# Kernel tuning notes

Hardware: AMD Instinct MI355X
Metric: run time of the kernel (lower is better)

## Reference

```python
import jax, jax.numpy as jnp
import numpy as np

N_NODES = 10000
N_EDGES = 320000
K_HOPS = 3
IN_CH = 128
OUT_CH = 128


def setup_inputs() -> dict:
    key = jax.random.key(0)
    k1, k2, k3, k4, k5 = jax.random.split(key, 5)
    h = jax.random.normal(k1, (N_NODES, IN_CH), dtype=jnp.float32)
    X = jax.random.normal(k2, (N_EDGES, K_HOPS), dtype=jnp.float32)
    edge_index = jax.random.randint(k3, (2, N_EDGES), 0, N_NODES, dtype=jnp.int64)
    batch_node = jax.random.uniform(k4, (N_NODES,), dtype=jnp.float32)
    # glorot init for weight, zeros for bias (matches reset_parameters)
    stdv = np.sqrt(6.0 / (IN_CH + OUT_CH))
    weight = jax.random.uniform(k5, (K_HOPS, IN_CH, OUT_CH), dtype=jnp.float32,
                                minval=-stdv, maxval=stdv)
    bias = jnp.zeros((OUT_CH,), dtype=jnp.float32)
    return {"h": h, "X": X, "edge_index": edge_index,
            "batch_node": batch_node, "weight": weight, "bias": bias}


def reference(h, X, edge_index, batch_node, weight, bias):
    # Original builds dense A[k, src, dst] = X[e, k] (zeros elsewhere), then
    # res = A @ h @ weight, max over k, + bias. We honor the sparsity:
    # agg[src, k, :] = sum_e X[e, k] * h[dst[e], :]  (sparse A @ h per hop k)
    n = batch_node.shape[0]
    src = edge_index[0]
    dst = edge_index[1]
    msg = X[:, :, None] * h[dst][:, None, :]                 # [E, K, in]
    agg = jax.ops.segment_sum(msg, src, num_segments=n)      # [N, K, in]
    res = jnp.einsum('nki,kio->kno', agg, weight)            # [K, N, out]
    out = res.max(axis=0) + bias                             # [N, out]
    return out
```

## Files before the change

kernel.cpp:

```cpp
#include <hip/hip_runtime.h>

#define N_NODES 10000
#define N_EDGES 320000
#define K_HOPS  3
#define CH      128
#define NBF     4
#define ROWP    136
#define SLOT    72

#define EDGE_BLKS 1250
#define HCV_BLKS  1250
#define WCV_BLKS  192

typedef __attribute__((ext_vector_type(8))) short  frag8;
typedef __attribute__((ext_vector_type(4))) float  floatx4;

__device__ inline unsigned short f2bf(float x) {
    union { float f; unsigned u; } v; v.f = x;
    unsigned r = v.u + 0x7fff + ((v.u >> 16) & 1);
    return (unsigned short)(r >> 16);
}

__global__ __launch_bounds__(256) void prep_fill_kernel(
    const float* __restrict__ h, const float* __restrict__ X,
    const int* __restrict__ ei, const float* __restrict__ W,
    unsigned short* __restrict__ hb, unsigned short* __restrict__ WT,
    int* __restrict__ cursor, float4* __restrict__ edata)
{
    int b = blockIdx.x;
    if (b < EDGE_BLKS) {
        int e = b * 256 + threadIdx.x;
        int src = ei[e];
        int dst = ei[N_EDGES + e];
        int r = atomicAdd(cursor + src, 1);
        if (r < SLOT)
            edata[(size_t)src * SLOT + r] =
                make_float4(X[e * K_HOPS + 0], X[e * K_HOPS + 1],
                            X[e * K_HOPS + 2], __int_as_float(dst));
    } else if (b < EDGE_BLKS + HCV_BLKS) {
        int tid = (b - EDGE_BLKS) * 256 + threadIdx.x;
        float4 v = *(const float4*)(h + (size_t)tid * 4);
        ushort4 p;
        p.x = f2bf(v.x); p.y = f2bf(v.y); p.z = f2bf(v.z); p.w = f2bf(v.w);
        *(ushort4*)(hb + (size_t)tid * 4) = p;
    } else {
        int tid = (b - EDGE_BLKS - HCV_BLKS) * 256 + threadIdx.x;
        int i = tid & 127;
        int o = (tid >> 7) & 127;
        int k = tid >> 14;
        WT[tid] = f2bf(W[((size_t)k * CH + i) * CH + o]);
    }
}

__device__ inline void hstep(const float4& ed, uint2 q, float (&a)[12]) {
    float h0 = __uint_as_float(q.x << 16);
    float h1 = __uint_as_float(q.x & 0xffff0000u);
    float h2 = __uint_as_float(q.y << 16);
    float h3 = __uint_as_float(q.y & 0xffff0000u);
    a[0] = fmaf(ed.x, h0, a[0]); a[1]  = fmaf(ed.x, h1, a[1]);
    a[2] = fmaf(ed.x, h2, a[2]); a[3]  = fmaf(ed.x, h3, a[3]);
    a[4] = fmaf(ed.y, h0, a[4]); a[5]  = fmaf(ed.y, h1, a[5]);
    a[6] = fmaf(ed.y, h2, a[6]); a[7]  = fmaf(ed.y, h3, a[7]);
    a[8] = fmaf(ed.z, h0, a[8]); a[9]  = fmaf(ed.z, h1, a[9]);
    a[10]= fmaf(ed.z, h2, a[10]); a[11]= fmaf(ed.z, h3, a[11]);
}

__global__ __launch_bounds__(256) void fused_kernel(
    const unsigned short* __restrict__ hb,
    const float4*         __restrict__ edata,
    const int*            __restrict__ counts,
    const unsigned short* __restrict__ WT,
    const float*          __restrict__ bias,
    float*                __restrict__ out)
{
    __shared__ unsigned short sA[K_HOPS][16][ROWP];
    const int node0 = blockIdx.x * NBF;
    const int t    = threadIdx.x;
    const int w    = t >> 6;
    const int lane = t & 63;
    const int half = lane >> 5;
    const int cq   = (lane & 31) * 4;

    const int n = node0 + w;
    const int cnt = __builtin_amdgcn_readfirstlane(min(counts[n], SLOT));
    const float4* ebase = edata + (size_t)n * SLOT;

#define HQ(ed) (*(const uint2*)(hb + ((size_t)__float_as_int((ed).w) << 7) + cq))

    float acc[12];
#pragma unroll
    for (int i = 0; i < 12; ++i) acc[i] = 0.f;

    const int full = cnt >> 1;
    int s = 0;
    for (; s + 4 <= full; s += 4) {
        float4 e0 = ebase[2 * (s + 0) + half];
        float4 e1 = ebase[2 * (s + 1) + half];
        float4 e2 = ebase[2 * (s + 2) + half];
        float4 e3 = ebase[2 * (s + 3) + half];
        uint2 q0 = HQ(e0), q1 = HQ(e1), q2 = HQ(e2), q3 = HQ(e3);
        hstep(e0, q0, acc); hstep(e1, q1, acc);
        hstep(e2, q2, acc); hstep(e3, q3, acc);
    }
    for (; s < full; ++s) {
        float4 e0 = ebase[2 * s + half];
        uint2 q0 = HQ(e0);
        hstep(e0, q0, acc);
    }
    if (cnt & 1) {
        float4 e0 = ebase[cnt - 1];
        uint2 q0 = HQ(e0);
        if (half) { e0.x = 0.f; e0.y = 0.f; e0.z = 0.f; }
        hstep(e0, q0, acc);
    }
#undef HQ

#pragma unroll
    for (int i = 0; i < 12; ++i) acc[i] += __shfl_xor(acc[i], 32, 64);

    if (half == 0) {
#pragma unroll
        for (int hop = 0; hop < K_HOPS; ++hop) {
            ushort4 p;
            p.x = f2bf(acc[4 * hop + 0]); p.y = f2bf(acc[4 * hop + 1]);
            p.z = f2bf(acc[4 * hop + 2]); p.w = f2bf(acc[4 * hop + 3]);
            *(ushort4*)&sA[hop][w][cq] = p;
        }
    }
    __syncthreads();

    const int col  = lane & 15;
    const int quad = lane >> 4;
    const int ob   = 32 * w;

    floatx4 m0 = {-3.4e38f, -3.4e38f, -3.4e38f, -3.4e38f};
    floatx4 m1 = m0;
#pragma unroll
    for (int hop = 0; hop < K_HOPS; ++hop) {
        floatx4 c0 = {0.f, 0.f, 0.f, 0.f};
        floatx4 c1 = {0.f, 0.f, 0.f, 0.f};
        const unsigned short* arow = &sA[hop][col][quad * 8];
        const unsigned short* b0p  = WT + ((size_t)hop * CH + ob + col) * CH + quad * 8;
        const unsigned short* b1p  = b0p + 16 * CH;
#pragma unroll
        for (int kt = 0; kt < 4; ++kt) {
            frag8 af  = *(const frag8*)(arow + kt * 32);
            frag8 bf0 = *(const frag8*)(b0p + kt * 32);
            frag8 bf1 = *(const frag8*)(b1p + kt * 32);
            c0 = __builtin_amdgcn_mfma_f32_16x16x32_bf16(af, bf0, c0, 0, 0, 0);
            c1 = __builtin_amdgcn_mfma_f32_16x16x32_bf16(af, bf1, c1, 0, 0, 0);
        }
#pragma unroll
        for (int r = 0; r < 4; ++r) {
            m0[r] = fmaxf(m0[r], c0[r]);
            m1[r] = fmaxf(m1[r], c1[r]);
        }
    }

    if (quad == 0) {
        const float bv0 = bias[ob + col];
        const float bv1 = bias[ob + 16 + col];
#pragma unroll
        for (int r = 0; r < 4; ++r) {
            out[(size_t)(node0 + r) * CH + ob + col]      = m0[r] + bv0;
            out[(size_t)(node0 + r) * CH + ob + 16 + col] = m1[r] + bv1;
        }
    }
}

extern "C" void kernel_launch(void* const* d_in, const int* in_sizes, int n_in,
                              void* d_out, int out_size, void* d_ws, size_t ws_size,
                              hipStream_t stream) {
    const float* h    = (const float*)d_in[0];
    const float* X    = (const float*)d_in[1];
    const int*   ei   = (const int*)  d_in[2];
    const float* W    = (const float*)d_in[4];
    const float* bias = (const float*)d_in[5];
    float*       out  = (float*)d_out;

    char* ws = (char*)d_ws;
    int* cursor = (int*)ws;                        ws += N_NODES * sizeof(int);
    unsigned short* hb = (unsigned short*)ws;      ws += (size_t)N_NODES * CH * sizeof(unsigned short);
    unsigned short* WT = (unsigned short*)ws;      ws += (size_t)K_HOPS * CH * CH * sizeof(unsigned short);
    ws = (char*)(((uintptr_t)ws + 15) & ~(uintptr_t)15);
    float4* edata = (float4*)ws;

    hipMemsetAsync(cursor, 0, N_NODES * sizeof(int), stream);

    prep_fill_kernel<<<EDGE_BLKS + HCV_BLKS + WCV_BLKS, 256, 0, stream>>>(
        h, X, ei, W, hb, WT, cursor, edata);
    fused_kernel<<<N_NODES / NBF, 256, 0, stream>>>(hb, edata, cursor, WT, bias, out);
}
```

Baseline: 135.7 us.

## Pack edge records to bf16, split atomic cursors, stage edges in LDS

Edge records shrink from a float4 to a uint2 holding the three bf16 hop weights and a 16-bit destination index. Each node's cursor is split into two padded sub-counters chosen by edge parity, which spreads out atomic contention and avoids false sharing. The fused kernel copies each node's edges into shared memory, zero-pads the tail, and gathers in unrolled groups of eight to expose more memory-level parallelism. In exchange it rounds the edge weights to bf16, enlarges the memset, and caps capacity at 44 edges per sub-slot.

```diff
diff --git a/kernel.cpp b/kernel.cpp
--- a/kernel.cpp
+++ b/kernel.cpp
@@ -6,7 +6,10 @@
 #define CH      128
 #define NBF     4
 #define ROWP    136
-#define SLOT    72
+#define SUBSLOT 44
+#define SLOT    88
+#define SEPAD   96
+#define CSTRIDE 16
 
 #define EDGE_BLKS 1250
 #define HCV_BLKS  1250
@@ -25,18 +28,23 @@
     const float* __restrict__ h, const float* __restrict__ X,
     const int* __restrict__ ei, const float* __restrict__ W,
     unsigned short* __restrict__ hb, unsigned short* __restrict__ WT,
-    int* __restrict__ cursor, float4* __restrict__ edata)
+    int* __restrict__ cursor, uint2* __restrict__ edata)
 {
     int b = blockIdx.x;
     if (b < EDGE_BLKS) {
         int e = b * 256 + threadIdx.x;
         int src = ei[e];
         int dst = ei[N_EDGES + e];
-        int r = atomicAdd(cursor + src, 1);
-        if (r < SLOT)
-            edata[(size_t)src * SLOT + r] =
-                make_float4(X[e * K_HOPS + 0], X[e * K_HOPS + 1],
-                            X[e * K_HOPS + 2], __int_as_float(dst));
+        int j = e & 1;
+        int r = atomicAdd(cursor + (2 * src + j) * CSTRIDE, 1);
+        if (r < SUBSLOT) {
+            uint2 rec;
+            rec.x = (unsigned)f2bf(X[e * K_HOPS + 0])
+                  | ((unsigned)f2bf(X[e * K_HOPS + 1]) << 16);
+            rec.y = (unsigned)f2bf(X[e * K_HOPS + 2])
+                  | ((unsigned)dst << 16);
+            edata[(size_t)src * SLOT + j * SUBSLOT + r] = rec;
+        }
     } else if (b < EDGE_BLKS + HCV_BLKS) {
         int tid = (b - EDGE_BLKS) * 256 + threadIdx.x;
         float4 v = *(const float4*)(h + (size_t)tid * 4);
@@ -52,28 +60,32 @@
     }
 }
 
-__device__ inline void hstep(const float4& ed, uint2 q, float (&a)[12]) {
+__device__ inline void estep(uint2 er, uint2 q, float (&a)[12]) {
+    float x0 = __uint_as_float(er.x << 16);
+    float x1 = __uint_as_float(er.x & 0xffff0000u);
+    float x2 = __uint_as_float(er.y << 16);
     float h0 = __uint_as_float(q.x << 16);
     float h1 = __uint_as_float(q.x & 0xffff0000u);
     float h2 = __uint_as_float(q.y << 16);
     float h3 = __uint_as_float(q.y & 0xffff0000u);
-    a[0] = fmaf(ed.x, h0, a[0]); a[1]  = fmaf(ed.x, h1, a[1]);
-    a[2] = fmaf(ed.x, h2, a[2]); a[3]  = fmaf(ed.x, h3, a[3]);
-    a[4] = fmaf(ed.y, h0, a[4]); a[5]  = fmaf(ed.y, h1, a[5]);
-    a[6] = fmaf(ed.y, h2, a[6]); a[7]  = fmaf(ed.y, h3, a[7]);
-    a[8] = fmaf(ed.z, h0, a[8]); a[9]  = fmaf(ed.z, h1, a[9]);
-    a[10]= fmaf(ed.z, h2, a[10]); a[11]= fmaf(ed.z, h3, a[11]);
+    a[0] = fmaf(x0, h0, a[0]); a[1]  = fmaf(x0, h1, a[1]);
+    a[2] = fmaf(x0, h2, a[2]); a[3]  = fmaf(x0, h3, a[3]);
+    a[4] = fmaf(x1, h0, a[4]); a[5]  = fmaf(x1, h1, a[5]);
+    a[6] = fmaf(x1, h2, a[6]); a[7]  = fmaf(x1, h3, a[7]);
+    a[8] = fmaf(x2, h0, a[8]); a[9]  = fmaf(x2, h1, a[9]);
+    a[10]= fmaf(x2, h2, a[10]); a[11]= fmaf(x2, h3, a[11]);
 }
 
 __global__ __launch_bounds__(256) void fused_kernel(
     const unsigned short* __restrict__ hb,
-    const float4*         __restrict__ edata,
-    const int*            __restrict__ counts,
+    const uint2*          __restrict__ edata,
+    const int*            __restrict__ cursor,
     const unsigned short* __restrict__ WT,
     const float*          __restrict__ bias,
     float*                __restrict__ out)
 {
     __shared__ unsigned short sA[K_HOPS][16][ROWP];
+    __shared__ uint2 sE[NBF][SEPAD];
     const int node0 = blockIdx.x * NBF;
     const int t    = threadIdx.x;
     const int w    = t >> 6;
@@ -82,38 +94,36 @@
     const int cq   = (lane & 31) * 4;
 
     const int n = node0 + w;
-    const int cnt = __builtin_amdgcn_readfirstlane(min(counts[n], SLOT));
-    const float4* ebase = edata + (size_t)n * SLOT;
-
-#define HQ(ed) (*(const uint2*)(hb + ((size_t)__float_as_int((ed).w) << 7) + cq))
+    int c0 = __builtin_amdgcn_readfirstlane(min(cursor[(2 * n + 0) * CSTRIDE], SUBSLOT));
+    int c1 = __builtin_amdgcn_readfirstlane(min(cursor[(2 * n + 1) * CSTRIDE], SUBSLOT));
+    const int cnt = c0 + c1;
+    const uint2* ebase = edata + (size_t)n * SLOT;
+
+    if (lane < c0) sE[w][lane] = ebase[lane];
+    if (lane < c1) sE[w][c0 + lane] = ebase[SUBSLOT + lane];
+    {
+        int z0 = cnt + lane, z1 = cnt + 64 + lane;
+        uint2 zz; zz.x = 0u; zz.y = 0u;
+        if (z0 < SEPAD) sE[w][z0] = zz;
+        if (z1 < SEPAD) sE[w][z1] = zz;
+    }
 
     float acc[12];
 #pragma unroll
     for (int i = 0; i < 12; ++i) acc[i] = 0.f;
 
-    const int full = cnt >> 1;
-    int s = 0;
-    for (; s + 4 <= full; s += 4) {
-        float4 e0 = ebase[2 * (s + 0) + half];
-        float4 e1 = ebase[2 * (s + 1) + half];
-        float4 e2 = ebase[2 * (s + 2) + half];
-        float4 e3 = ebase[2 * (s + 3) + half];
-        uint2 q0 = HQ(e0), q1 = HQ(e1), q2 = HQ(e2), q3 = HQ(e3);
-        hstep(e0, q0, acc); hstep(e1, q1, acc);
-        hstep(e2, q2, acc); hstep(e3, q3, acc);
-    }
-    for (; s < full; ++s) {
-        float4 e0 = ebase[2 * s + half];
-        uint2 q0 = HQ(e0);
-        hstep(e0, q0, acc);
-    }
-    if (cnt & 1) {
-        float4 e0 = ebase[cnt - 1];
-        uint2 q0 = HQ(e0);
-        if (half) { e0.x = 0.f; e0.y = 0.f; e0.z = 0.f; }
-        hstep(e0, q0, acc);
-    }
-#undef HQ
+    const int groups = (cnt + 15) >> 4;
+    for (int g = 0; g < groups; ++g) {
+        const int s = g * 8;
+        uint2 er[8], q[8];
+#pragma unroll
+        for (int k = 0; k < 8; ++k) er[k] = sE[w][2 * (s + k) + half];
+#pragma unroll
+        for (int k = 0; k < 8; ++k)
+            q[k] = *(const uint2*)(hb + ((size_t)(er[k].y >> 16) << 7) + cq);
+#pragma unroll
+        for (int k = 0; k < 8; ++k) estep(er[k], q[k], acc);
+    }
 
 #pragma unroll
     for (int i = 0; i < 12; ++i) acc[i] += __shfl_xor(acc[i], 32, 64);
@@ -137,8 +147,8 @@
     floatx4 m1 = m0;
 #pragma unroll
     for (int hop = 0; hop < K_HOPS; ++hop) {
-        floatx4 c0 = {0.f, 0.f, 0.f, 0.f};
-        floatx4 c1 = {0.f, 0.f, 0.f, 0.f};
+        floatx4 c0v = {0.f, 0.f, 0.f, 0.f};
+        floatx4 c1v = {0.f, 0.f, 0.f, 0.f};
         const unsigned short* arow = &sA[hop][col][quad * 8];
         const unsigned short* b0p  = WT + ((size_t)hop * CH + ob + col) * CH + quad * 8;
         const unsigned short* b1p  = b0p + 16 * CH;
@@ -147,13 +157,13 @@
             frag8 af  = *(const frag8*)(arow + kt * 32);
             frag8 bf0 = *(const frag8*)(b0p + kt * 32);
             frag8 bf1 = *(const frag8*)(b1p + kt * 32);
-            c0 = __builtin_amdgcn_mfma_f32_16x16x32_bf16(af, bf0, c0, 0, 0, 0);
-            c1 = __builtin_amdgcn_mfma_f32_16x16x32_bf16(af, bf1, c1, 0, 0, 0);
+            c0v = __builtin_amdgcn_mfma_f32_16x16x32_bf16(af, bf0, c0v, 0, 0, 0);
+            c1v = __builtin_amdgcn_mfma_f32_16x16x32_bf16(af, bf1, c1v, 0, 0, 0);
         }
 #pragma unroll
         for (int r = 0; r < 4; ++r) {
-            m0[r] = fmaxf(m0[r], c0[r]);
-            m1[r] = fmaxf(m1[r], c1[r]);
+            m0[r] = fmaxf(m0[r], c0v[r]);
+            m1[r] = fmaxf(m1[r], c1v[r]);
         }
     }
 
@@ -179,13 +189,12 @@
     float*       out  = (float*)d_out;
 
     char* ws = (char*)d_ws;
-    int* cursor = (int*)ws;                        ws += N_NODES * sizeof(int);
+    int* cursor = (int*)ws;                        ws += (size_t)N_NODES * 2 * CSTRIDE * sizeof(int);
     unsigned short* hb = (unsigned short*)ws;      ws += (size_t)N_NODES * CH * sizeof(unsigned short);
     unsigned short* WT = (unsigned short*)ws;      ws += (size_t)K_HOPS * CH * CH * sizeof(unsigned short);
-    ws = (char*)(((uintptr_t)ws + 15) & ~(uintptr_t)15);
-    float4* edata = (float4*)ws;
-
-    hipMemsetAsync(cursor, 0, N_NODES * sizeof(int), stream);
+    uint2* edata = (uint2*)ws;
+
+    hipMemsetAsync(cursor, 0, (size_t)N_NODES * 2 * CSTRIDE * sizeof(int), stream);
 
     prep_fill_kernel<<<EDGE_BLKS + HCV_BLKS + WCV_BLKS, 256, 0, stream>>>(
         h, X, ei, W, hb, WT, cursor, edata);
```

After: 125.5 us. 1.08x faster.
